# Kernel optimization log

Hardware: AMD Instinct MI355X
Metric: run time of the kernel (lower is better)

Reference implementation:

```python
import jax, jax.numpy as jnp
import numpy as np

N_NODES = 100000
N_EDGES = 800000
IN_DIM, HID_DIM, OUT_DIM = 128, 256, 128


def setup_inputs() -> dict:
    key = jax.random.key(0)
    ks = jax.random.split(key, 8)
    x = jax.random.normal(ks[0], (N_NODES, IN_DIM), dtype=jnp.float32)
    edge_index = jax.random.randint(ks[1], (2, N_EDGES), 0, N_NODES, dtype=jnp.int32)
    s = lambda k, shp, fan_in: jax.random.normal(k, shp, dtype=jnp.float32) / np.sqrt(fan_in)
    return {
        "x": x,
        "edge_index": edge_index,
        "W1_l": s(ks[2], (HID_DIM, IN_DIM), IN_DIM),   # applied to aggregated neighbors
        "b1": jnp.zeros((HID_DIM,), jnp.float32),
        "W1_r": s(ks[3], (HID_DIM, IN_DIM), IN_DIM),   # root/self transform (no bias, as in PyG)
        "W2_l": s(ks[4], (OUT_DIM, HID_DIM), HID_DIM),
        "b2": jnp.zeros((OUT_DIM,), jnp.float32),
        "W2_r": s(ks[5], (OUT_DIM, HID_DIM), HID_DIM),
    }


def _sage_conv(x, src, dst, W_l, b, W_r):
    # mean aggregation of source-neighbor features onto targets
    msg = x[src]                                              # [E, d]
    agg = jax.ops.segment_sum(msg, dst, num_segments=N_NODES)  # [N, d]
    cnt = jax.ops.segment_sum(jnp.ones((src.shape[0],), x.dtype), dst, num_segments=N_NODES)
    mean = agg / jnp.maximum(cnt, 1.0)[:, None]
    # SAGEConv: lin_l(aggr) + lin_r(x)
    return mean @ W_l.T + b + x @ W_r.T


def reference(x, edge_index, W1_l, b1, W1_r, W2_l, b2, W2_r):
    src, dst = edge_index[0], edge_index[1]
    h = jax.nn.relu(_sage_conv(x, src, dst, W1_l, b1, W1_r))
    # dropout p=0.0 -> identity (eval-mode equivalent)
    out = _sage_conv(h, src, dst, W2_l, b2, W2_r)
    return out
```

## Files before the change

kernel.cpp:

```cpp
#include <hip/hip_runtime.h>

#define NN 100000
#define NE 800000

typedef __attribute__((ext_vector_type(4))) float f32x4;
typedef __attribute__((ext_vector_type(4))) int   i32x4;
typedef __attribute__((ext_vector_type(8))) unsigned short u16x8;

__device__ __forceinline__ unsigned short f2bf(float f) {
  unsigned u = __float_as_uint(f);
  return (unsigned short)((u + 0x7FFFu + ((u >> 16) & 1u)) >> 16);
}
__device__ __forceinline__ float bf2f(unsigned short b) {
  return __uint_as_float(((unsigned)b) << 16);
}

__global__ void degree_k(const int* __restrict__ dst, int* __restrict__ deg,
                         int* __restrict__ rord) {
  int e = blockIdx.x * 256 + threadIdx.x;
  if (e < NE) rord[e] = atomicAdd(&deg[dst[e]], 1);
}

__global__ __launch_bounds__(256) void scan1_k(const int* __restrict__ deg,
    int* __restrict__ offs, int* __restrict__ bsum, float* __restrict__ inv) {
  __shared__ int s[256];
  int t = threadIdx.x;
  int base = blockIdx.x * 1024 + t * 4;
  int v[4], tsum = 0;
#pragma unroll
  for (int k = 0; k < 4; ++k) {
    int i = base + k;
    v[k] = (i < NN) ? deg[i] : 0;
    tsum += v[k];
    if (i < NN) inv[i] = 1.0f / fmaxf((float)v[k], 1.0f);
  }
  s[t] = tsum; __syncthreads();
  int val = tsum;
#pragma unroll
  for (int off = 1; off < 256; off <<= 1) {
    int x = (t >= off) ? s[t - off] : 0;
    __syncthreads();
    val += x; s[t] = val;
    __syncthreads();
  }
  int excl = val - tsum;
  if (t == 255) bsum[blockIdx.x] = val;
  int run = excl;
#pragma unroll
  for (int k = 0; k < 4; ++k) { int i = base + k; if (i < NN) offs[i] = run; run += v[k]; }
}

__global__ __launch_bounds__(256) void scan2_k(int* __restrict__ bsum, int nb) {
  __shared__ int s[256];
  int t = threadIdx.x;
  int v = (t < nb) ? bsum[t] : 0;
  s[t] = v; __syncthreads();
  int val = v;
#pragma unroll
  for (int off = 1; off < 256; off <<= 1) {
    int x = (t >= off) ? s[t - off] : 0;
    __syncthreads();
    val += x; s[t] = val;
    __syncthreads();
  }
  if (t < nb) bsum[t] = val - v;
}

__global__ __launch_bounds__(256) void scan3_k(int* __restrict__ offs,
    const int* __restrict__ bsum) {
  int base = blockIdx.x * 1024 + threadIdx.x * 4;
  int add = bsum[blockIdx.x];
#pragma unroll
  for (int k = 0; k < 4; ++k) {
    int i = base + k;
    if (i < NN) offs[i] += add;
  }
}

__global__ void fill_k(const int* __restrict__ src, const int* __restrict__ dst,
    const int* __restrict__ offs, const int* __restrict__ rord,
    int* __restrict__ eidx) {
  int e = blockIdx.x * 256 + threadIdx.x;
  if (e < NE) {
    int p = offs[dst[e]] + rord[e];
    __builtin_nontemporal_store(src[e], &eidx[p]);
  }
}

__global__ __launch_bounds__(256) void cast_x_k(const float* __restrict__ in,
    unsigned short* __restrict__ outb) {
  int i = blockIdx.x * 256 + threadIdx.x;
  if (i >= NN * 128 / 4) return;
  float4 v = *reinterpret_cast<const float4*>(in + (size_t)i * 4);
  ushort4 o;
  o.x = f2bf(v.x); o.y = f2bf(v.y); o.z = f2bf(v.z); o.w = f2bf(v.w);
  *reinterpret_cast<ushort4*>(outb + (size_t)i * 4) = o;
}

__global__ __launch_bounds__(256) void cast_w4_k(const float* __restrict__ Wa,
    const float* __restrict__ Wb, const float* __restrict__ Wc,
    const float* __restrict__ Wd, unsigned short* __restrict__ outb) {
  int i = blockIdx.x * 256 + threadIdx.x;
  if (i >= 4 * 32768) return;
  int seg = i >> 15, off = i & 32767;
  const float* s = (seg < 2) ? (seg == 0 ? Wa : Wb) : (seg == 2 ? Wc : Wd);
  outb[i] = f2bf(s[off]);
}

template<int GMODE>
__global__ __launch_bounds__(256) void gather_k(const unsigned short* __restrict__ feat,
    const int* __restrict__ offs, const int* __restrict__ deg,
    const float* __restrict__ inv, const int* __restrict__ eidx,
    const unsigned short* __restrict__ selfb,
    unsigned short* __restrict__ outb, float* __restrict__ outf) {
  int node = blockIdx.x * 16 + (threadIdx.x >> 4);
  int l = threadIdx.x & 15;
  if (node >= NN) return;
  int st = offs[node], n = deg[node];
  float a[8];
#pragma unroll
  for (int k = 0; k < 8; ++k) a[k] = 0.f;

  int j = 0;
  for (; j + 4 <= n; j += 4) {
    int s0 = eidx[st + j + 0];
    int s1 = eidx[st + j + 1];
    int s2 = eidx[st + j + 2];
    int s3 = eidx[st + j + 3];
    u16x8 r0 = *reinterpret_cast<const u16x8*>(feat + (size_t)s0 * 128 + l * 8);
    u16x8 r1 = *reinterpret_cast<const u16x8*>(feat + (size_t)s1 * 128 + l * 8);
    u16x8 r2 = *reinterpret_cast<const u16x8*>(feat + (size_t)s2 * 128 + l * 8);
    u16x8 r3 = *reinterpret_cast<const u16x8*>(feat + (size_t)s3 * 128 + l * 8);
#pragma unroll
    for (int k = 0; k < 8; ++k)
      a[k] += (bf2f(r0[k]) + bf2f(r1[k])) + (bf2f(r2[k]) + bf2f(r3[k]));
  }
  for (; j < n; ++j) {
    int s = eidx[st + j];
    u16x8 r = *reinterpret_cast<const u16x8*>(feat + (size_t)s * 128 + l * 8);
#pragma unroll
    for (int k = 0; k < 8; ++k) a[k] += bf2f(r[k]);
  }

  float sc = inv[node];
  if (GMODE == 2) {
    u16x8 sb = *reinterpret_cast<const u16x8*>(selfb + (size_t)node * 128 + l * 8);
    float4 o0, o1;
    o0.x = bf2f(sb[0]) + sc * a[0]; o0.y = bf2f(sb[1]) + sc * a[1];
    o0.z = bf2f(sb[2]) + sc * a[2]; o0.w = bf2f(sb[3]) + sc * a[3];
    o1.x = bf2f(sb[4]) + sc * a[4]; o1.y = bf2f(sb[5]) + sc * a[5];
    o1.z = bf2f(sb[6]) + sc * a[6]; o1.w = bf2f(sb[7]) + sc * a[7];
    float* po = outf + (size_t)node * 128 + l * 8;
    *reinterpret_cast<float4*>(po) = o0;
    *reinterpret_cast<float4*>(po + 4) = o1;
  } else {
    u16x8 o;
#pragma unroll
    for (int k = 0; k < 8; ++k) o[k] = f2bf(sc * a[k]);
    *reinterpret_cast<u16x8*>(outb + (size_t)node * 128 + l * 8) = o;
  }
}

template<int MODE>
__global__ __launch_bounds__(256, 2) void mgemm_k(
    const unsigned short* __restrict__ A1, const unsigned short* __restrict__ A2,
    const unsigned short* __restrict__ Wbase, const float* __restrict__ bias,
    unsigned short* __restrict__ outb, unsigned short* __restrict__ outb2) {
  __shared__ unsigned short As[2][64 * 256];
  const int t = threadIdx.x;
  const int wave = t >> 6, lane = t & 63;
  const int lhi = lane >> 4, llo = lane & 15;

  i32x4 bfrag[8][4];
  float bv[4];
#pragma unroll
  for (int fn = 0; fn < 4; ++fn) {
    int c = wave * 64 + fn * 16 + llo;
    const unsigned short* rowp;
    if (MODE == 0) {
      rowp = Wbase + (size_t)c * 128;
      bv[fn] = bias[c];
    } else {
      rowp = Wbase + (wave >= 2 ? 32768 : 0) + (size_t)(c & 127) * 256;
      bv[fn] = (wave >= 2) ? bias[c & 127] : 0.f;
    }
#pragma unroll
    for (int ks = 0; ks < 8; ++ks) {
      int koff = (MODE == 0) ? ((ks & 3) * 32 + lhi * 8 + ((ks >= 4) ? 32768 : 0))
                             : (ks * 32 + lhi * 8);
      bfrag[ks][fn] = *reinterpret_cast<const i32x4*>(rowp + koff);
    }
  }

  auto stage = [&](int buf, int row0) {
#pragma unroll
    for (int c = 0; c < 8; ++c) {
      int chunk = wave * 8 + c;
      int tb = chunk * 1024 + lane * 16;
      int r = tb >> 9;
      int cb = tb & 511;
      int cbs = cb ^ ((r & 7) << 4);
      int gr = min(row0 + r, NN - 1);
      const char* gsrc;
      if (MODE == 0) {
        const unsigned short* Asel = (cbs < 256) ? A1 : A2;
        gsrc = (const char*)(Asel + (size_t)gr * 128) + (cbs & 255);
      } else {
        gsrc = (const char*)(A1 + (size_t)gr * 256) + cbs;
      }
      __builtin_amdgcn_global_load_lds(
          (const __attribute__((address_space(1))) void*)gsrc,
          (__attribute__((address_space(3))) void*)((char*)As + buf * 32768 + chunk * 1024),
          16, 0, 0);
    }
  };

  const int npan = (NN + 63) >> 6;
  int p = blockIdx.x;
  stage(0, p * 64);
  int cur = 0;

#pragma unroll 1
  for (; p < npan; p += gridDim.x) {
    int pn = p + gridDim.x;
    if (pn < npan) stage(cur ^ 1, pn * 64);
    asm volatile("s_waitcnt vmcnt(8)" ::: "memory");
    __builtin_amdgcn_s_barrier();

    const int row0 = p * 64;
    f32x4 acc[4][4];
#pragma unroll
    for (int fm = 0; fm < 4; ++fm)
#pragma unroll
      for (int fn = 0; fn < 4; ++fn) acc[fm][fn] = (f32x4)0.f;

#pragma unroll
    for (int ks = 0; ks < 8; ++ks) {
      i32x4 a[4];
#pragma unroll
      for (int fm = 0; fm < 4; ++fm) {
        int r = fm * 16 + llo;
        int cb = (ks * 64 + lhi * 16) ^ ((r & 7) << 4);
        a[fm] = *reinterpret_cast<const i32x4*>((const char*)As + cur * 32768 + r * 512 + cb);
      }
#pragma unroll
      for (int fm = 0; fm < 4; ++fm)
#pragma unroll
        for (int fn = 0; fn < 4; ++fn)
          asm("v_mfma_f32_16x16x32_bf16 %0, %1, %2, %0"
              : "+v"(acc[fm][fn]) : "v"(a[fm]), "v"(bfrag[ks][fn]));
    }

    asm volatile("s_nop 7\n\ts_nop 7");

#pragma unroll
    for (int fm = 0; fm < 4; ++fm) {
#pragma unroll
      for (int fn = 0; fn < 4; ++fn) {
        int col = wave * 64 + fn * 16 + llo;
#pragma unroll
        for (int j = 0; j < 4; ++j) {
          int row = row0 + fm * 16 + lhi * 4 + j;
          if (row < NN) {
            float v = acc[fm][fn][j] + bv[fn];
            if (MODE == 0) {
              v = fmaxf(v, 0.f);
              outb[(size_t)row * 256 + col] = f2bf(v);
            } else if (wave < 2) {
              outb[(size_t)row * 128 + col] = f2bf(v);
            } else {
              outb2[(size_t)row * 128 + (col - 128)] = f2bf(v);
            }
          }
        }
      }
    }
    __builtin_amdgcn_s_barrier();
    cur ^= 1;
  }
}

extern "C" void kernel_launch(void* const* d_in, const int* in_sizes, int n_in,
                              void* d_out, int out_size, void* d_ws, size_t ws_size,
                              hipStream_t stream) {
  const float* x   = (const float*)d_in[0];
  const int*   ei  = (const int*)d_in[1];
  const float* W1l = (const float*)d_in[2];
  const float* b1  = (const float*)d_in[3];
  const float* W1r = (const float*)d_in[4];
  const float* W2l = (const float*)d_in[5];
  const float* b2  = (const float*)d_in[6];
  const float* W2r = (const float*)d_in[7];
  float* out = (float*)d_out;

  char* ws = (char*)d_ws;
  float*          inv    = (float*)(ws);
  int*            deg    = (int*)(ws + 0x80000);
  int*            offs   = (int*)(ws + 0x100000);
  int*            bsum   = (int*)(ws + 0x200000);
  unsigned short* Wb     = (unsigned short*)(ws + 0x280000);
  int*            eidx   = (int*)(ws + 0x400000);
  unsigned short* xb     = (unsigned short*)(ws + 0x800000);
  unsigned short* m1b    = (unsigned short*)(ws + 0x2200000);
  unsigned short* hb     = (unsigned short*)(ws + 0x3C00000);
  unsigned short* hWb    = (unsigned short*)(ws + 0x6E00000);
  int*            rord   = (int*)(ws + 0x8600000);
  unsigned short* selfb  = m1b;

  const int* src = ei;
  const int* dst = ei + NE;
  const int NB = (NN + 1023) / 1024;

  hipMemsetAsync(deg, 0, NN * sizeof(int), stream);
  degree_k<<<(NE + 255) / 256, 256, 0, stream>>>(dst, deg, rord);
  scan1_k<<<NB, 256, 0, stream>>>(deg, offs, bsum, inv);
  scan2_k<<<1, 256, 0, stream>>>(bsum, NB);
  scan3_k<<<NB, 256, 0, stream>>>(offs, bsum);
  fill_k<<<(NE + 255) / 256, 256, 0, stream>>>(src, dst, offs, rord, eidx);

  cast_x_k<<<(NN * 128 / 4 + 255) / 256, 256, 0, stream>>>(x, xb);
  cast_w4_k<<<(4 * 32768 + 255) / 256, 256, 0, stream>>>(W1l, W1r, W2l, W2r, Wb);

  gather_k<0><<<(NN + 15) / 16, 256, 0, stream>>>(xb, offs, deg, inv, eidx, nullptr, m1b, nullptr);
  mgemm_k<0><<<512, 256, 0, stream>>>(m1b, xb, Wb, b1, hb, nullptr);

  mgemm_k<1><<<512, 256, 0, stream>>>(hb, nullptr, Wb + 65536, b2, hWb, selfb);
  gather_k<2><<<(NN + 15) / 16, 256, 0, stream>>>(hWb, offs, deg, inv, eidx, selfb, nullptr, out);
}
```

Baseline: 226.3 us.

## Fuse layer-1 neighbor mean gather into the layer-1 GEMM panel staging

The first-layer mean aggregation is computed inside the GEMM kernel. Each thread gathers one quarter of a node's row and writes the scaled bf16 result into swizzled shared memory, while the self features stream in through async LDS loads. This removes the separate gather launch and the global write and re-read of the intermediate mean matrix. In exchange the gather now runs with only 4 lanes per node and 32-float accumulators, so it has less memory-level parallelism and more register pressure. The full vmcnt(0) wait also leaves less gather latency overlapped with the MFMA work.

```diff
diff --git a/kernel.cpp b/kernel.cpp
--- a/kernel.cpp
+++ b/kernel.cpp
@@ -107,12 +107,10 @@
   outb[i] = f2bf(s[off]);
 }
 
-template<int GMODE>
-__global__ __launch_bounds__(256) void gather_k(const unsigned short* __restrict__ feat,
+__global__ __launch_bounds__(256) void gather2_k(const unsigned short* __restrict__ feat,
     const int* __restrict__ offs, const int* __restrict__ deg,
     const float* __restrict__ inv, const int* __restrict__ eidx,
-    const unsigned short* __restrict__ selfb,
-    unsigned short* __restrict__ outb, float* __restrict__ outf) {
+    const unsigned short* __restrict__ selfb, float* __restrict__ outf) {
   int node = blockIdx.x * 16 + (threadIdx.x >> 4);
   int l = threadIdx.x & 15;
   if (node >= NN) return;
@@ -143,27 +141,166 @@
   }
 
   float sc = inv[node];
-  if (GMODE == 2) {
-    u16x8 sb = *reinterpret_cast<const u16x8*>(selfb + (size_t)node * 128 + l * 8);
-    float4 o0, o1;
-    o0.x = bf2f(sb[0]) + sc * a[0]; o0.y = bf2f(sb[1]) + sc * a[1];
-    o0.z = bf2f(sb[2]) + sc * a[2]; o0.w = bf2f(sb[3]) + sc * a[3];
-    o1.x = bf2f(sb[4]) + sc * a[4]; o1.y = bf2f(sb[5]) + sc * a[5];
-    o1.z = bf2f(sb[6]) + sc * a[6]; o1.w = bf2f(sb[7]) + sc * a[7];
-    float* po = outf + (size_t)node * 128 + l * 8;
-    *reinterpret_cast<float4*>(po) = o0;
-    *reinterpret_cast<float4*>(po + 4) = o1;
-  } else {
-    u16x8 o;
-#pragma unroll
-    for (int k = 0; k < 8; ++k) o[k] = f2bf(sc * a[k]);
-    *reinterpret_cast<u16x8*>(outb + (size_t)node * 128 + l * 8) = o;
-  }
-}
-
-template<int MODE>
-__global__ __launch_bounds__(256, 2) void mgemm_k(
-    const unsigned short* __restrict__ A1, const unsigned short* __restrict__ A2,
+  u16x8 sb = *reinterpret_cast<const u16x8*>(selfb + (size_t)node * 128 + l * 8);
+  float4 o0, o1;
+  o0.x = bf2f(sb[0]) + sc * a[0]; o0.y = bf2f(sb[1]) + sc * a[1];
+  o0.z = bf2f(sb[2]) + sc * a[2]; o0.w = bf2f(sb[3]) + sc * a[3];
+  o1.x = bf2f(sb[4]) + sc * a[4]; o1.y = bf2f(sb[5]) + sc * a[5];
+  o1.z = bf2f(sb[6]) + sc * a[6]; o1.w = bf2f(sb[7]) + sc * a[7];
+  float* po = outf + (size_t)node * 128 + l * 8;
+  *reinterpret_cast<float4*>(po) = o0;
+  *reinterpret_cast<float4*>(po + 4) = o1;
+}
+
+__global__ __launch_bounds__(256, 2) void fgemm1_k(
+    const unsigned short* __restrict__ xb,
+    const int* __restrict__ offs, const int* __restrict__ deg,
+    const float* __restrict__ inv, const int* __restrict__ eidx,
+    const unsigned short* __restrict__ Wbase, const float* __restrict__ bias,
+    unsigned short* __restrict__ outb) {
+  __shared__ unsigned short Am1[2][64 * 128];
+  __shared__ unsigned short Asf[2][64 * 128];
+  const int t = threadIdx.x;
+  const int wave = t >> 6, lane = t & 63;
+  const int lhi = lane >> 4, llo = lane & 15;
+
+  i32x4 bfrag[8][4];
+  float bv[4];
+#pragma unroll
+  for (int fn = 0; fn < 4; ++fn) {
+    int c = wave * 64 + fn * 16 + llo;
+    const unsigned short* rowp = Wbase + (size_t)c * 128;
+    bv[fn] = bias[c];
+#pragma unroll
+    for (int ks = 0; ks < 8; ++ks) {
+      int koff = (ks & 3) * 32 + lhi * 8 + ((ks >= 4) ? 32768 : 0);
+      bfrag[ks][fn] = *reinterpret_cast<const i32x4*>(rowp + koff);
+    }
+  }
+
+  const int gn = t >> 2;
+  const int gl = t & 3;
+
+  auto stage = [&](int buf, int p) {
+    const int row0 = p * 64;
+#pragma unroll
+    for (int c = 0; c < 4; ++c) {
+      int chunk = wave * 4 + c;
+      int tb = chunk * 1024 + lane * 16;
+      int r = tb >> 8;
+      int cb = tb & 255;
+      int cbs = cb ^ ((r & 7) << 4);
+      int gr = min(row0 + r, NN - 1);
+      __builtin_amdgcn_global_load_lds(
+          (const __attribute__((address_space(1))) void*)
+              ((const char*)(xb + (size_t)gr * 128) + cbs),
+          (__attribute__((address_space(3))) void*)((char*)&Asf[buf][0] + chunk * 1024),
+          16, 0, 0);
+    }
+    int node = row0 + gn;
+    bool valid = node < NN;
+    int st = 0, cnt = 0;
+    float sc = 0.f;
+    if (valid) { st = offs[node]; cnt = deg[node]; sc = inv[node]; }
+    float a[32];
+#pragma unroll
+    for (int k = 0; k < 32; ++k) a[k] = 0.f;
+    const unsigned short* fb = xb + gl * 32;
+    int j = 0;
+    for (; j + 2 <= cnt; j += 2) {
+      int s0 = eidx[st + j], s1 = eidx[st + j + 1];
+      const u16x8* p0 = reinterpret_cast<const u16x8*>(fb + (size_t)s0 * 128);
+      const u16x8* p1 = reinterpret_cast<const u16x8*>(fb + (size_t)s1 * 128);
+      u16x8 r0[4], r1[4];
+#pragma unroll
+      for (int q = 0; q < 4; ++q) { r0[q] = p0[q]; r1[q] = p1[q]; }
+#pragma unroll
+      for (int q = 0; q < 4; ++q)
+#pragma unroll
+        for (int k = 0; k < 8; ++k)
+          a[q * 8 + k] += bf2f(r0[q][k]) + bf2f(r1[q][k]);
+    }
+    if (j < cnt) {
+      int s0 = eidx[st + j];
+      const u16x8* p0 = reinterpret_cast<const u16x8*>(fb + (size_t)s0 * 128);
+#pragma unroll
+      for (int q = 0; q < 4; ++q) {
+        u16x8 r0 = p0[q];
+#pragma unroll
+        for (int k = 0; k < 8; ++k) a[q * 8 + k] += bf2f(r0[k]);
+      }
+    }
+#pragma unroll
+    for (int q = 0; q < 4; ++q) {
+      u16x8 o;
+#pragma unroll
+      for (int k = 0; k < 8; ++k) o[k] = f2bf(sc * a[q * 8 + k]);
+      int addr = gn * 256 + ((gl * 64 + q * 16) ^ ((gn & 7) << 4));
+      *reinterpret_cast<u16x8*>((char*)&Am1[buf][0] + addr) = o;
+    }
+  };
+
+  const int npan = (NN + 63) >> 6;
+  int p = blockIdx.x;
+  stage(0, p);
+  int cur = 0;
+
+#pragma unroll 1
+  for (; p < npan; p += gridDim.x) {
+    int pn = p + gridDim.x;
+    if (pn < npan) stage(cur ^ 1, pn);
+    asm volatile("s_waitcnt vmcnt(0) lgkmcnt(0)" ::: "memory");
+    __builtin_amdgcn_s_barrier();
+
+    const int row0 = p * 64;
+    f32x4 acc[4][4];
+#pragma unroll
+    for (int fm = 0; fm < 4; ++fm)
+#pragma unroll
+      for (int fn = 0; fn < 4; ++fn) acc[fm][fn] = (f32x4)0.f;
+
+#pragma unroll
+    for (int ks = 0; ks < 8; ++ks) {
+      const char* half = (ks < 4) ? (const char*)&Am1[cur][0] : (const char*)&Asf[cur][0];
+      i32x4 a[4];
+#pragma unroll
+      for (int fm = 0; fm < 4; ++fm) {
+        int r = fm * 16 + llo;
+        int cb = (((ks & 3) * 64 + lhi * 16)) ^ ((r & 7) << 4);
+        a[fm] = *reinterpret_cast<const i32x4*>(half + r * 256 + cb);
+      }
+#pragma unroll
+      for (int fm = 0; fm < 4; ++fm)
+#pragma unroll
+        for (int fn = 0; fn < 4; ++fn)
+          asm("v_mfma_f32_16x16x32_bf16 %0, %1, %2, %0"
+              : "+v"(acc[fm][fn]) : "v"(a[fm]), "v"(bfrag[ks][fn]));
+    }
+
+    asm volatile("s_nop 7\n\ts_nop 7");
+
+#pragma unroll
+    for (int fm = 0; fm < 4; ++fm) {
+#pragma unroll
+      for (int fn = 0; fn < 4; ++fn) {
+        int col = wave * 64 + fn * 16 + llo;
+#pragma unroll
+        for (int j = 0; j < 4; ++j) {
+          int row = row0 + fm * 16 + lhi * 4 + j;
+          if (row < NN) {
+            float v = fmaxf(acc[fm][fn][j] + bv[fn], 0.f);
+            outb[(size_t)row * 256 + col] = f2bf(v);
+          }
+        }
+      }
+    }
+    __builtin_amdgcn_s_barrier();
+    cur ^= 1;
+  }
+}
+
+__global__ __launch_bounds__(256, 2) void mgemm2_k(
+    const unsigned short* __restrict__ A1,
     const unsigned short* __restrict__ Wbase, const float* __restrict__ bias,
     unsigned short* __restrict__ outb, unsigned short* __restrict__ outb2) {
   __shared__ unsigned short As[2][64 * 256];
@@ -176,20 +313,11 @@
 #pragma unroll
   for (int fn = 0; fn < 4; ++fn) {
     int c = wave * 64 + fn * 16 + llo;
-    const unsigned short* rowp;
-    if (MODE == 0) {
-      rowp = Wbase + (size_t)c * 128;
-      bv[fn] = bias[c];
-    } else {
-      rowp = Wbase + (wave >= 2 ? 32768 : 0) + (size_t)(c & 127) * 256;
-      bv[fn] = (wave >= 2) ? bias[c & 127] : 0.f;
-    }
-#pragma unroll
-    for (int ks = 0; ks < 8; ++ks) {
-      int koff = (MODE == 0) ? ((ks & 3) * 32 + lhi * 8 + ((ks >= 4) ? 32768 : 0))
-                             : (ks * 32 + lhi * 8);
-      bfrag[ks][fn] = *reinterpret_cast<const i32x4*>(rowp + koff);
-    }
+    const unsigned short* rowp = Wbase + (wave >= 2 ? 32768 : 0) + (size_t)(c & 127) * 256;
+    bv[fn] = (wave >= 2) ? bias[c & 127] : 0.f;
+#pragma unroll
+    for (int ks = 0; ks < 8; ++ks)
+      bfrag[ks][fn] = *reinterpret_cast<const i32x4*>(rowp + ks * 32 + lhi * 8);
   }
 
   auto stage = [&](int buf, int row0) {
@@ -201,15 +329,9 @@
       int cb = tb & 511;
       int cbs = cb ^ ((r & 7) << 4);
       int gr = min(row0 + r, NN - 1);
-      const char* gsrc;
-      if (MODE == 0) {
-        const unsigned short* Asel = (cbs < 256) ? A1 : A2;
-        gsrc = (const char*)(Asel + (size_t)gr * 128) + (cbs & 255);
-      } else {
-        gsrc = (const char*)(A1 + (size_t)gr * 256) + cbs;
-      }
       __builtin_amdgcn_global_load_lds(
-          (const __attribute__((address_space(1))) void*)gsrc,
+          (const __attribute__((address_space(1))) void*)
+              ((const char*)(A1 + (size_t)gr * 256) + cbs),
           (__attribute__((address_space(3))) void*)((char*)As + buf * 32768 + chunk * 1024),
           16, 0, 0);
     }
@@ -263,14 +385,8 @@
           int row = row0 + fm * 16 + lhi * 4 + j;
           if (row < NN) {
             float v = acc[fm][fn][j] + bv[fn];
-            if (MODE == 0) {
-              v = fmaxf(v, 0.f);
-              outb[(size_t)row * 256 + col] = f2bf(v);
-            } else if (wave < 2) {
-              outb[(size_t)row * 128 + col] = f2bf(v);
-            } else {
-              outb2[(size_t)row * 128 + (col - 128)] = f2bf(v);
-            }
+            if (wave < 2) outb[(size_t)row * 128 + col] = f2bf(v);
+            else          outb2[(size_t)row * 128 + (col - 128)] = f2bf(v);
           }
         }
       }
@@ -301,11 +417,10 @@
   unsigned short* Wb     = (unsigned short*)(ws + 0x280000);
   int*            eidx   = (int*)(ws + 0x400000);
   unsigned short* xb     = (unsigned short*)(ws + 0x800000);
-  unsigned short* m1b    = (unsigned short*)(ws + 0x2200000);
+  unsigned short* selfb  = (unsigned short*)(ws + 0x2200000);
   unsigned short* hb     = (unsigned short*)(ws + 0x3C00000);
   unsigned short* hWb    = (unsigned short*)(ws + 0x6E00000);
   int*            rord   = (int*)(ws + 0x8600000);
-  unsigned short* selfb  = m1b;
 
   const int* src = ei;
   const int* dst = ei + NE;
@@ -321,9 +436,8 @@
   cast_x_k<<<(NN * 128 / 4 + 255) / 256, 256, 0, stream>>>(x, xb);
   cast_w4_k<<<(4 * 32768 + 255) / 256, 256, 0, stream>>>(W1l, W1r, W2l, W2r, Wb);
 
-  gather_k<0><<<(NN + 15) / 16, 256, 0, stream>>>(xb, offs, deg, inv, eidx, nullptr, m1b, nullptr);
-  mgemm_k<0><<<512, 256, 0, stream>>>(m1b, xb, Wb, b1, hb, nullptr);
-
-  mgemm_k<1><<<512, 256, 0, stream>>>(hb, nullptr, Wb + 65536, b2, hWb, selfb);
-  gather_k<2><<<(NN + 15) / 16, 256, 0, stream>>>(hWb, offs, deg, inv, eidx, selfb, nullptr, out);
-}
+  fgemm1_k<<<512, 256, 0, stream>>>(xb, offs, deg, inv, eidx, Wb, b1, hb);
+
+  mgemm2_k<<<512, 256, 0, stream>>>(hb, Wb + 65536, b2, hWb, selfb);
+  gather2_k<<<(NN + 15) / 16, 256, 0, stream>>>(hWb, offs, deg, inv, eidx, selfb, out);
+}
```

New measurement: 228.9 us. About the same (+1.2%).
